# Performance work log

Hardware: AMD Instinct MI355X
Metric: run time of the kernel (lower is better)

## Reference

```python
import jax, jax.numpy as jnp
import numpy as np

B, T, HID = 1, 2048, 2048
H = 16            # num_heads == num_key_value_heads
D = HID // H      # head_dim == feature_dim == 128
EPS = 1e-5


def _layer_norm(x, eps=1e-5):
    mu = jnp.mean(x, axis=-1, keepdims=True)
    var = jnp.mean((x - mu) ** 2, axis=-1, keepdims=True)
    return (x - mu) * jax.lax.rsqrt(var + eps)


def _feature_map(x, gamma, beta):
    # ReBased feature map, flatten=False (parallel mode): affine then LayerNorm
    return _layer_norm(x * gamma + beta)


def setup_inputs() -> dict:
    key = jax.random.key(0)
    ks = jax.random.split(key, 8)
    s = HID ** -0.5
    return {
        "hidden_states": jax.random.normal(ks[0], (B, T, HID), jnp.float32),
        "Wq": jax.random.normal(ks[1], (HID, HID), jnp.float32) * s,
        "Wk": jax.random.normal(ks[2], (HID, HID), jnp.float32) * s,
        "Wv": jax.random.normal(ks[3], (HID, HID), jnp.float32) * s,
        "Wo": jax.random.normal(ks[4], (HID, HID), jnp.float32) * s,
        "gamma": 1.0 + 0.1 * jax.random.normal(ks[5], (D,), jnp.float32),
        "beta": 0.1 * jax.random.normal(ks[6], (D,), jnp.float32),
    }


def reference(hidden_states, Wq, Wk, Wv, Wo, gamma, beta):
    b, t, _ = hidden_states.shape
    # projections (nn.Linear: x @ W.T), split into heads: [b, t, h, d]
    q = (hidden_states @ Wq.T).reshape(b, t, H, D)
    k = (hidden_states @ Wk.T).reshape(b, t, H, D)
    v = (hidden_states @ Wv.T).reshape(b, t, H, D)
    # ReBased feature map (no quadratic flatten in parallel mode)
    q = _feature_map(q, gamma, beta)
    k = _feature_map(k, gamma, beta)
    # parallel_rebased: scale q, quadratic score, causal mask, normalize
    q = q * (D ** -0.5)
    attn = jnp.einsum('bqhd,bkhd->bhqk', q, k) ** 2  # (q.k)^2
    mask = jnp.tril(jnp.ones((t, t), dtype=bool))
    attn = jnp.where(mask, attn, 0.0)
    o = jnp.einsum('bhqk,bkhd->bqhd', attn, v)       # [b, t, h, d]
    z = jnp.sum(attn, axis=-1)                       # [b, h, t]
    o = o / (jnp.swapaxes(z, 1, 2)[..., None] + EPS)
    o = o.reshape(b, t, H * D)
    return o @ Wo.T
```

## Files before the change

kernel.cpp:

```cpp
#include <hip/hip_runtime.h>
#include <hip/hip_bf16.h>
#include <stdint.h>

typedef __bf16 bf16;
typedef __bf16 v8bf __attribute__((ext_vector_type(8)));
typedef float  v4f  __attribute__((ext_vector_type(4)));

#define TSEQ   2048
#define HIDDIM 2048
#define NHEAD  16
#define HDIM   128

__device__ __forceinline__ void async16(void* lds, const void* g)
{
    __builtin_amdgcn_global_load_lds(
        (__attribute__((address_space(1))) void*)(uintptr_t)g,
        (__attribute__((address_space(3))) void*)(unsigned int)(uintptr_t)lds,
        16, 0, 0);
}

__global__ __launch_bounds__(256) void conv5(const float* __restrict__ s0, bf16* __restrict__ d0,
                                             const float* __restrict__ s1, bf16* __restrict__ d1,
                                             const float* __restrict__ s2, bf16* __restrict__ d2,
                                             const float* __restrict__ s3, bf16* __restrict__ d3,
                                             const float* __restrict__ s4, bf16* __restrict__ d4)
{
    const float* src; bf16* dst;
    switch (blockIdx.y) {
        case 0: src = s0; dst = d0; break;
        case 1: src = s1; dst = d1; break;
        case 2: src = s2; dst = d2; break;
        case 3: src = s3; dst = d3; break;
        default: src = s4; dst = d4; break;
    }
    const size_t i = ((size_t)blockIdx.x * 256 + threadIdx.x) * 8;
    const float4 a = *(const float4*)(src + i);
    const float4 b = *(const float4*)(src + i + 4);
    v8bf o;
    o[0] = (bf16)a.x; o[1] = (bf16)a.y; o[2] = (bf16)a.z; o[3] = (bf16)a.w;
    o[4] = (bf16)b.x; o[5] = (bf16)b.y; o[6] = (bf16)b.z; o[7] = (bf16)b.w;
    *(v8bf*)(dst + i) = o;
}


#define PBAR() do { __builtin_amdgcn_sched_barrier(0); __builtin_amdgcn_s_barrier(); \
                    __builtin_amdgcn_sched_barrier(0); } while (0)

#define STU(ldst, gsrc) do { \
    async16((ldst) + w*512,        (gsrc) + (size_t)(w*8 + (l>>3))*2048); \
    async16((ldst) + 4096 + w*512, (gsrc) + (size_t)(64 + w*8 + (l>>3))*2048); \
} while (0)

#define RDA(buf) do { _Pragma("unroll") \
    for (int mi_ = 0; mi_ < 4; ++mi_) { \
        const bf16* p_ = &sA[(buf)*8192 + (wm*64 + mi_*16 + lr)*64]; \
        a[mi_][0] = *(const v8bf*)(p_ + c0); \
        a[mi_][1] = *(const v8bf*)(p_ + c1); } } while (0)

#define RDB(buf, nh) do { _Pragma("unroll") \
    for (int nj_ = 0; nj_ < 2; ++nj_) { \
        const bf16* p_ = &sB[(buf)*24576 + ((nh)*128 + wn*32 + nj_*16 + lr)*64]; \
        b[nj_][0] = *(const v8bf*)(p_ + c0); \
        b[nj_][1] = *(const v8bf*)(p_ + c1); } } while (0)

#define MQ(nh) do { _Pragma("unroll") \
    for (int mi_ = 0; mi_ < 4; ++mi_) { _Pragma("unroll") \
        for (int nj_ = 0; nj_ < 2; ++nj_) { \
            acc[mi_][(nh)*2+nj_] = __builtin_amdgcn_mfma_f32_16x16x32_bf16( \
                a[mi_][0], b[nj_][0], acc[mi_][(nh)*2+nj_], 0, 0, 0); \
            acc[mi_][(nh)*2+nj_] = __builtin_amdgcn_mfma_f32_16x16x32_bf16( \
                a[mi_][1], b[nj_][1], acc[mi_][(nh)*2+nj_], 0, 0, 0); \
        } } } while (0)

#define VMC(n) asm volatile("s_waitcnt vmcnt(" #n ")" ::: "memory")

__global__ __launch_bounds__(512, 2) void gemm_qkv384(const bf16* __restrict__ A,
    const bf16* __restrict__ Wcat, bf16* __restrict__ qb, bf16* __restrict__ kb,
    bf16* __restrict__ vb)
{
    __shared__ __attribute__((aligned(16))) bf16 sA[2*8192];
    __shared__ __attribute__((aligned(16))) bf16 sB[2*24576];
    const int n0g = blockIdx.x * 384;
    const int m0  = blockIdx.y * 128;

    const int tid = threadIdx.x, l = tid & 63, w = tid >> 6;
    const int wm = w >> 2, wn = w & 3;
    const int quad = l >> 4, lr = l & 15;
    const int scol = ((l & 7) ^ ((l >> 3) & 7)) * 8;
    const int c0 = ((quad    ) ^ (lr & 7)) * 8;
    const int c1 = ((quad + 4) ^ (lr & 7)) * 8;

    const bf16* Ag = A    + (size_t)m0  * 2048 + scol;
    const bf16* Bg = Wcat + (size_t)n0g * 2048 + scol;

    v4f  acc[4][6] = {};
    v8bf a[4][2], b[2][2];

    STU(&sA[0],           Ag);
    STU(&sB[0],           Bg);
    STU(&sB[8192],        Bg + (size_t)128*2048);
    STU(&sB[16384],       Bg + (size_t)256*2048);
    STU(&sA[8192],        Ag + 64);
    STU(&sB[24576],       Bg + 64);
    STU(&sB[24576+8192],  Bg + (size_t)128*2048 + 64);
    VMC(10);
    __builtin_amdgcn_s_barrier();
    __builtin_amdgcn_sched_barrier(0);

#pragma unroll 1
    for (int it = 0; it < 16; ++it) {
        const int k1 =  it*128 + 64;
        const int k2 = (it*128 + 128) & 2047;
        const int k3 = (it*128 + 192) & 2047;

        RDA(0); RDB(0, 0);
        STU(&sB[24576+16384], Bg + (size_t)256*2048 + k1);
        PBAR(); __builtin_amdgcn_s_setprio(1); MQ(0); __builtin_amdgcn_s_setprio(0);
        VMC(10); PBAR();
        RDB(0, 1);
        STU(&sA[0], Ag + k2);
        STU(&sB[0], Bg + k2);
        PBAR(); __builtin_amdgcn_s_setprio(1); MQ(1); __builtin_amdgcn_s_setprio(0);
        VMC(12); PBAR();
        RDB(0, 2);
        STU(&sB[8192], Bg + (size_t)128*2048 + k2);
        PBAR(); __builtin_amdgcn_s_setprio(1); MQ(2); __builtin_amdgcn_s_setprio(0);
        VMC(10); PBAR();
        RDA(1); RDB(1, 0);
        STU(&sB[16384], Bg + (size_t)256*2048 + k2);
        PBAR(); __builtin_amdgcn_s_setprio(1); MQ(0); __builtin_amdgcn_s_setprio(0);
        VMC(10); PBAR();
        RDB(1, 1);
        STU(&sA[8192],  Ag + k3);
        STU(&sB[24576], Bg + k3);
        PBAR(); __builtin_amdgcn_s_setprio(1); MQ(1); __builtin_amdgcn_s_setprio(0);
        VMC(12); PBAR();
        RDB(1, 2);
        STU(&sB[24576+8192], Bg + (size_t)128*2048 + k3);
        PBAR(); __builtin_amdgcn_s_setprio(1); MQ(2); __builtin_amdgcn_s_setprio(0);
        VMC(10); PBAR();
    }
    asm volatile("s_waitcnt vmcnt(0)" ::: "memory");

#pragma unroll
    for (int mi = 0; mi < 4; ++mi) {
        const int row = m0 + wm*64 + mi*16 + quad*4;
#pragma unroll
        for (int j = 0; j < 6; ++j) {
            const int colg  = n0g + (j >> 1)*128 + wn*32 + (j & 1)*16;
            const int which = colg >> 11;
            bf16* Cb = (which == 0) ? qb : (which == 1) ? kb : vb;
            const int lcol = (colg & 2047) + lr;
#pragma unroll
            for (int r = 0; r < 4; ++r)
                Cb[(size_t)(row + r)*2048 + lcol] = (bf16)acc[mi][j][r];
        }
    }
}

__global__ __launch_bounds__(256) void gemm_out(const bf16* __restrict__ A,
    const bf16* __restrict__ B, float* __restrict__ C)
{
    __shared__ __attribute__((aligned(16))) bf16 sA[128*32];
    __shared__ __attribute__((aligned(16))) bf16 sB[64*32];
    const int m0 = blockIdx.y * 128, n0 = blockIdx.x * 64;
    const int K = HIDDIM, ldc = HIDDIM;
    const int tid  = threadIdx.x;
    const int lane = tid & 63;
    const int w    = tid >> 6;
    const int wm   = w >> 1, wn = w & 1;
    const int quad = lane >> 4, lr = lane & 15;
    const int srow = lane >> 2;
    const int scol = (lane & 3) * 8;

    const bf16* gA0 = A + (size_t)(m0 + w*32 + srow) * K + scol;
    const bf16* gB0 = B + (size_t)(n0 + w*16 + srow) * K + scol;
    bf16* lA0 = &sA[w*1024];
    bf16* lB0 = &sB[w*512];

    v4f acc[4][2] = {};

    for (int kt = 0; kt < K; kt += 32) {
        __syncthreads();
        async16(lA0,       gA0 + kt);
        async16(lA0 + 512, gA0 + (size_t)16*K + kt);
        async16(lB0,       gB0 + kt);
        __syncthreads();
        v8bf a[4], b[2];
#pragma unroll
        for (int i = 0; i < 4; ++i)
            a[i] = *(const v8bf*)&sA[(wm*64 + i*16 + lr)*32 + quad*8];
#pragma unroll
        for (int j = 0; j < 2; ++j)
            b[j] = *(const v8bf*)&sB[(wn*32 + j*16 + lr)*32 + quad*8];
#pragma unroll
        for (int i = 0; i < 4; ++i)
#pragma unroll
            for (int j = 0; j < 2; ++j)
                acc[i][j] = __builtin_amdgcn_mfma_f32_16x16x32_bf16(a[i], b[j], acc[i][j], 0, 0, 0);
    }

#pragma unroll
    for (int i = 0; i < 4; ++i) {
        const int row_b = m0 + wm*64 + i*16 + quad*4;
#pragma unroll
        for (int j = 0; j < 2; ++j) {
            const int col = n0 + wn*32 + j*16 + lr;
#pragma unroll
            for (int r = 0; r < 4; ++r)
                C[(size_t)(row_b + r)*ldc + col] = acc[i][j][r];
        }
    }
}

__global__ __launch_bounds__(256) void fmap(bf16* __restrict__ qb, bf16* __restrict__ kb,
                                            const float* __restrict__ gamma,
                                            const float* __restrict__ beta)
{
    const int rid  = blockIdx.x * 4 + (threadIdx.x >> 6);
    const int lane = threadIdx.x & 63;
    bf16* base = (rid < TSEQ*NHEAD) ? (qb + (size_t)rid * HDIM)
                                    : (kb + (size_t)(rid - TSEQ*NHEAD) * HDIM);
    const float scale = (rid < TSEQ*NHEAD) ? 0.08838834764831845f : 1.0f;

    const bf16 x0b = base[lane*2], x1b = base[lane*2+1];
    const float g0 = gamma[lane*2], g1 = gamma[lane*2+1];
    const float b0 = beta[lane*2],  b1 = beta[lane*2+1];
    float x0 = (float)x0b*g0 + b0;
    float x1 = (float)x1b*g1 + b1;
    float s  = x0 + x1;
    float sq = x0*x0 + x1*x1;
#pragma unroll
    for (int off = 1; off < 64; off <<= 1) { s += __shfl_xor(s, off); sq += __shfl_xor(sq, off); }
    const float mu   = s * (1.0f/128.0f);
    float var        = sq * (1.0f/128.0f) - mu*mu;
    var = fmaxf(var, 0.0f);
    const float rstd = rsqrtf(var + 1e-5f);
    base[lane*2]   = (bf16)((x0 - mu) * rstd * scale);
    base[lane*2+1] = (bf16)((x1 - mu) * rstd * scale);
}

__global__ __launch_bounds__(256) void transpose2048(const bf16* __restrict__ src,
                                                     bf16* __restrict__ dst)
{
    __shared__ __attribute__((aligned(16))) bf16 tile[64][72];
    const int t0 = blockIdx.y * 64, c0 = blockIdx.x * 64;
    const int tid = threadIdx.x;
    const int r = tid >> 3;
    const int c = (tid & 7) * 8;
#pragma unroll
    for (int p = 0; p < 2; ++p) {
        const int rr = r + p*32;
        *(v8bf*)&tile[rr][c] = *(const v8bf*)(src + (size_t)(t0+rr)*HIDDIM + c0 + c);
    }
    __syncthreads();
#pragma unroll
    for (int p = 0; p < 2; ++p) {
        const int orow = r + p*32;
        v8bf o;
#pragma unroll
        for (int i = 0; i < 8; ++i) o[i] = tile[c + i][orow];
        *(v8bf*)(dst + (size_t)(c0+orow)*HIDDIM + t0 + c) = o;
    }
}

__global__ __launch_bounds__(512, 2) void attn(const bf16* __restrict__ qb,
                                               const bf16* __restrict__ kb,
                                               const bf16* __restrict__ vt,
                                               bf16* __restrict__ ob)
{
    __shared__ __attribute__((aligned(16))) bf16 sK[2*64*136];
    __shared__ __attribute__((aligned(16))) bf16 sV[2*128*72];
    __shared__ __attribute__((aligned(16))) bf16 sS[2*64*72];
    __shared__ __attribute__((aligned(16))) float sO[64*129];
    __shared__ __attribute__((aligned(16))) float sZ[64*17];

    const int h    = blockIdx.y;
    const int pr   = blockIdx.x;
    const int tid  = threadIdx.x, lane = tid & 63;
    const int w    = tid >> 6;
    const int g    = w >> 2;
    const int ww   = w & 3;
    const int quad = lane >> 4, lr = lane & 15;
    const int rs   = tid >> 4;
    const int cs   = (tid & 15) * 8;

#pragma unroll
    for (int ti = 0; ti < 2; ++ti) {
        const int tile = ti ? pr : (31 - pr);
        const int nch  = tile + 1;

        v8bf qa[4];
        {
            const bf16* q0 = qb + (size_t)(tile*64 + ww*16 + lr)*HIDDIM + h*HDIM + quad*8;
#pragma unroll
            for (int ks = 0; ks < 4; ++ks)
                qa[ks] = *(const v8bf*)(q0 + ks*32);
        }

        v4f  o[8] = {};
        float z[4] = {0.f, 0.f, 0.f, 0.f};

        v8bf curK[4], curV[4], nxtK[4], nxtV[4];
#pragma unroll
        for (int p = 0; p < 4; ++p) {
            curK[p] = *(const v8bf*)(kb + (size_t)(rs + p*32)*HIDDIM + h*HDIM + cs);
            curV[p] = *(const v8bf*)(vt + (size_t)(h*HDIM + rs + p*32)*HIDDIM + cs);
        }

        for (int ich = 0; ich < nch; ich += 2) {
            __syncthreads();
#pragma unroll
            for (int p = 0; p < 4; ++p) {
                const int r = rs + p*32;
                *(v8bf*)&sK[(r>>6)*8704 + (r&63)*136 + cs] = curK[p];
            }
#pragma unroll
            for (int p = 0; p < 4; ++p)
                *(v8bf*)&sV[(cs>>6)*9216 + (rs + p*32)*72 + (cs & 63)] = curV[p];

            if (ich + 2 < nch) {
                const int s1 = (ich + 2) * 64;
#pragma unroll
                for (int p = 0; p < 4; ++p) {
                    nxtK[p] = *(const v8bf*)(kb + (size_t)(s1 + rs + p*32)*HIDDIM + h*HDIM + cs);
                    nxtV[p] = *(const v8bf*)(vt + (size_t)(h*HDIM + rs + p*32)*HIDDIM + s1 + cs);
                }
            }
            __syncthreads();

            const int ch = ich + g;
            if (ch < nch) {
                const bf16* sKg = &sK[g*8704];
                const bf16* sVg = &sV[g*9216];
                bf16*       sSg = &sS[g*4608];
                const bool  diag = (ch == tile);
                const int   s0   = ch * 64;

                v8bf kbf[4][4];
#pragma unroll
                for (int nj = 0; nj < 4; ++nj)
#pragma unroll
                    for (int ks = 0; ks < 4; ++ks)
                        kbf[nj][ks] = *(const v8bf*)&sKg[(nj*16 + lr)*136 + ks*32 + quad*8];
                const int row_l = ww*16 + quad*4;
                const int qg    = tile*64 + row_l;
#pragma unroll
                for (int nj = 0; nj < 4; ++nj) {
                    v4f s4 = {0.f, 0.f, 0.f, 0.f};
#pragma unroll
                    for (int ks = 0; ks < 4; ++ks)
                        s4 = __builtin_amdgcn_mfma_f32_16x16x32_bf16(qa[ks], kbf[nj][ks], s4, 0, 0, 0);
                    const int col = nj*16 + lr;
                    const int sg  = s0 + col;
#pragma unroll
                    for (int r = 0; r < 4; ++r) {
                        float val = s4[r] * s4[r];
                        if (diag && (sg > qg + r)) val = 0.0f;
                        const bf16 vb16 = (bf16)val;
                        z[r] += (float)vb16;
                        sSg[(row_l + r)*72 + col] = vb16;
                    }
                }

#pragma unroll
                for (int ks = 0; ks < 2; ++ks) {
                    const v8bf sa = *(const v8bf*)&sSg[(ww*16 + lr)*72 + ks*32 + quad*8];
#pragma unroll
                    for (int nd = 0; nd < 8; ++nd) {
                        const v8bf vbf = *(const v8bf*)&sVg[(nd*16 + lr)*72 + ks*32 + quad*8];
                        o[nd] = __builtin_amdgcn_mfma_f32_16x16x32_bf16(sa, vbf, o[nd], 0, 0, 0);
                    }
                }
            }

            if (ich + 2 < nch) {
#pragma unroll
                for (int p = 0; p < 4; ++p) { curK[p] = nxtK[p]; curV[p] = nxtV[p]; }
            }
        }

        const int row_l = ww*16 + quad*4;
        __syncthreads();
        if (g == 1) {
#pragma unroll
            for (int nd = 0; nd < 8; ++nd)
#pragma unroll
                for (int r = 0; r < 4; ++r)
                    sO[(row_l + r)*129 + nd*16 + lr] = o[nd][r];
#pragma unroll
            for (int r = 0; r < 4; ++r)
                sZ[(row_l + r)*17 + lr] = z[r];
        }
        __syncthreads();
        if (g == 0) {
#pragma unroll
            for (int nd = 0; nd < 8; ++nd)
#pragma unroll
                for (int r = 0; r < 4; ++r)
                    o[nd][r] += sO[(row_l + r)*129 + nd*16 + lr];
#pragma unroll
            for (int r = 0; r < 4; ++r) {
                float zz = z[r] + sZ[(row_l + r)*17 + lr];
                zz += __shfl_xor(zz, 1); zz += __shfl_xor(zz, 2);
                zz += __shfl_xor(zz, 4); zz += __shfl_xor(zz, 8);
                z[r] = zz + 1e-5f;
            }
            const size_t rbase = (size_t)(tile*64 + row_l)*HIDDIM + h*HDIM;
#pragma unroll
            for (int nd = 0; nd < 8; ++nd) {
                const int col = nd*16 + lr;
#pragma unroll
                for (int r = 0; r < 4; ++r)
                    ob[rbase + (size_t)r*HIDDIM + col] = (bf16)(o[nd][r] / z[r]);
            }
        }
    }
}

extern "C" void kernel_launch(void* const* d_in, const int* in_sizes, int n_in,
                              void* d_out, int out_size, void* d_ws, size_t ws_size,
                              hipStream_t stream)
{
    const float* hs    = (const float*)d_in[0];
    const float* Wq    = (const float*)d_in[1];
    const float* Wk    = (const float*)d_in[2];
    const float* Wv    = (const float*)d_in[3];
    const float* Wo    = (const float*)d_in[4];
    const float* gamma = (const float*)d_in[5];
    const float* beta  = (const float*)d_in[6];
    float* outp = (float*)d_out;

    const size_t MAT = (size_t)TSEQ * HIDDIM;

    bf16* ws   = (bf16*)d_ws;
    bf16* hs_b = ws + 0*MAT;
    bf16* vt   = hs_b;
    bf16* Wq_b = ws + 1*MAT;
    bf16* Wk_b = ws + 2*MAT;
    bf16* Wv_b = ws + 3*MAT;
    bf16* Wo_b = ws + 4*MAT;
    bf16* vb   = ws + 5*MAT;
    bf16* ob   = vb;
    bf16* qb   = (bf16*)d_out;
    bf16* kb   = (bf16*)d_out + MAT;

    conv5<<<dim3(2048, 5), 256, 0, stream>>>(hs, hs_b, Wq, Wq_b, Wk, Wk_b, Wv, Wv_b, Wo, Wo_b);
    gemm_qkv384<<<dim3(16, 16), 512, 0, stream>>>(hs_b, Wq_b, qb, kb, vb);
    fmap<<<dim3(2*TSEQ*NHEAD/4), 256, 0, stream>>>(qb, kb, gamma, beta);
    transpose2048<<<dim3(32, 32), 256, 0, stream>>>(vb, vt);
    attn<<<dim3(16, 16), 512, 0, stream>>>(qb, kb, vt, ob);
    gemm_out<<<dim3(32, 16), 256, 0, stream>>>(ob, Wo_b, outp);
}
```

Measured before the change: 269.4 us.

## Fuse feature-map LayerNorm and V transpose into QKV GEMM epilogue

The QKV projection epilogue now applies the affine-plus-LayerNorm feature map to Q and K tiles, using shuffle reductions and an LDS cross-wave reduction over each 128-wide head. It also writes V directly in transposed layout. This removes the separate fmap and transpose kernels together with their global memory round trips and launches. In exchange the GEMM epilogue gains extra LDS traffic and syncs, and the transposed V stores are strided 8-byte writes.

```diff
diff --git a/kernel.cpp b/kernel.cpp
--- a/kernel.cpp
+++ b/kernel.cpp
@@ -4,6 +4,7 @@
 
 typedef __bf16 bf16;
 typedef __bf16 v8bf __attribute__((ext_vector_type(8)));
+typedef __bf16 v4bf __attribute__((ext_vector_type(4)));
 typedef float  v4f  __attribute__((ext_vector_type(4)));
 
 #define TSEQ   2048
@@ -76,7 +77,7 @@
 
 __global__ __launch_bounds__(512, 2) void gemm_qkv384(const bf16* __restrict__ A,
     const bf16* __restrict__ Wcat, bf16* __restrict__ qb, bf16* __restrict__ kb,
-    bf16* __restrict__ vb)
+    bf16* __restrict__ vt, const float* __restrict__ gamma, const float* __restrict__ beta)
 {
     __shared__ __attribute__((aligned(16))) bf16 sA[2*8192];
     __shared__ __attribute__((aligned(16))) bf16 sB[2*24576];
@@ -141,19 +142,88 @@
         VMC(10); PBAR();
     }
     asm volatile("s_waitcnt vmcnt(0)" ::: "memory");
+    __syncthreads();
+
+    float* sRed = (float*)sA;
+    const float g0f = gamma[wn*32 + lr],      b0f = beta[wn*32 + lr];
+    const float g1f = gamma[wn*32 + 16 + lr], b1f = beta[wn*32 + 16 + lr];
+
+#pragma unroll
+    for (int nh = 0; nh < 3; ++nh) {
+        if (((n0g + nh*128) >> 11) == 2) continue;
+#pragma unroll
+        for (int mi = 0; mi < 4; ++mi) {
+            float s[4] = {0.f,0.f,0.f,0.f}, sq[4] = {0.f,0.f,0.f,0.f};
+#pragma unroll
+            for (int jj = 0; jj < 2; ++jj) {
+                const float gg = jj ? g1f : g0f, bb = jj ? b1f : b0f;
+#pragma unroll
+                for (int r = 0; r < 4; ++r) {
+                    float x = acc[mi][nh*2+jj][r] * gg + bb;
+                    acc[mi][nh*2+jj][r] = x;
+                    s[r] += x; sq[r] += x*x;
+                }
+            }
+#pragma unroll
+            for (int off = 1; off < 16; off <<= 1)
+#pragma unroll
+                for (int r = 0; r < 4; ++r) {
+                    s[r]  += __shfl_xor(s[r],  off);
+                    sq[r] += __shfl_xor(sq[r], off);
+                }
+            if (lr == 0) {
+#pragma unroll
+                for (int r = 0; r < 4; ++r) {
+                    const int row = wm*64 + mi*16 + quad*4 + r;
+                    float* p = &sRed[((nh*128 + row)*5 + wn)*2];
+                    p[0] = s[r]; p[1] = sq[r];
+                }
+            }
+        }
+    }
+    __syncthreads();
 
 #pragma unroll
     for (int mi = 0; mi < 4; ++mi) {
         const int row = m0 + wm*64 + mi*16 + quad*4;
-#pragma unroll
-        for (int j = 0; j < 6; ++j) {
-            const int colg  = n0g + (j >> 1)*128 + wn*32 + (j & 1)*16;
+        const int rl0 = wm*64 + mi*16 + quad*4;
+#pragma unroll
+        for (int nh = 0; nh < 3; ++nh) {
+            const int colg  = n0g + nh*128 + wn*32;
             const int which = colg >> 11;
-            bf16* Cb = (which == 0) ? qb : (which == 1) ? kb : vb;
-            const int lcol = (colg & 2047) + lr;
-#pragma unroll
-            for (int r = 0; r < 4; ++r)
-                Cb[(size_t)(row + r)*2048 + lcol] = (bf16)acc[mi][j][r];
+            if (which == 2) {
+#pragma unroll
+                for (int jj = 0; jj < 2; ++jj) {
+                    const int c = (colg & 2047) + jj*16 + lr;
+                    v4bf pk;
+#pragma unroll
+                    for (int r = 0; r < 4; ++r) pk[r] = (bf16)acc[mi][nh*2+jj][r];
+                    *(v4bf*)(vt + (size_t)c*2048 + row) = pk;
+                }
+            } else {
+                bf16* Cb = (which == 0) ? qb : kb;
+                const float qs = (which == 0) ? 0.08838834764831845f : 1.0f;
+#pragma unroll
+                for (int r = 0; r < 4; ++r) {
+                    const int rl = rl0 + r;
+                    float S = 0.f, Q = 0.f;
+#pragma unroll
+                    for (int t = 0; t < 4; ++t) {
+                        const float* p = &sRed[((nh*128 + rl)*5 + t)*2];
+                        S += p[0]; Q += p[1];
+                    }
+                    const float mu = S * (1.0f/128.0f);
+                    float var = Q * (1.0f/128.0f) - mu*mu;
+                    var = fmaxf(var, 0.0f);
+                    const float rstd = rsqrtf(var + 1e-5f) * qs;
+#pragma unroll
+                    for (int jj = 0; jj < 2; ++jj) {
+                        const int lcol = (colg & 2047) + jj*16 + lr;
+                        Cb[(size_t)(row + r)*2048 + lcol] =
+                            (bf16)((acc[mi][nh*2+jj][r] - mu) * rstd);
+                    }
+                }
+            }
         }
     }
 }
@@ -213,57 +283,6 @@
     }
 }
 
-__global__ __launch_bounds__(256) void fmap(bf16* __restrict__ qb, bf16* __restrict__ kb,
-                                            const float* __restrict__ gamma,
-                                            const float* __restrict__ beta)
-{
-    const int rid  = blockIdx.x * 4 + (threadIdx.x >> 6);
-    const int lane = threadIdx.x & 63;
-    bf16* base = (rid < TSEQ*NHEAD) ? (qb + (size_t)rid * HDIM)
-                                    : (kb + (size_t)(rid - TSEQ*NHEAD) * HDIM);
-    const float scale = (rid < TSEQ*NHEAD) ? 0.08838834764831845f : 1.0f;
-
-    const bf16 x0b = base[lane*2], x1b = base[lane*2+1];
-    const float g0 = gamma[lane*2], g1 = gamma[lane*2+1];
-    const float b0 = beta[lane*2],  b1 = beta[lane*2+1];
-    float x0 = (float)x0b*g0 + b0;
-    float x1 = (float)x1b*g1 + b1;
-    float s  = x0 + x1;
-    float sq = x0*x0 + x1*x1;
-#pragma unroll
-    for (int off = 1; off < 64; off <<= 1) { s += __shfl_xor(s, off); sq += __shfl_xor(sq, off); }
-    const float mu   = s * (1.0f/128.0f);
-    float var        = sq * (1.0f/128.0f) - mu*mu;
-    var = fmaxf(var, 0.0f);
-    const float rstd = rsqrtf(var + 1e-5f);
-    base[lane*2]   = (bf16)((x0 - mu) * rstd * scale);
-    base[lane*2+1] = (bf16)((x1 - mu) * rstd * scale);
-}
-
-__global__ __launch_bounds__(256) void transpose2048(const bf16* __restrict__ src,
-                                                     bf16* __restrict__ dst)
-{
-    __shared__ __attribute__((aligned(16))) bf16 tile[64][72];
-    const int t0 = blockIdx.y * 64, c0 = blockIdx.x * 64;
-    const int tid = threadIdx.x;
-    const int r = tid >> 3;
-    const int c = (tid & 7) * 8;
-#pragma unroll
-    for (int p = 0; p < 2; ++p) {
-        const int rr = r + p*32;
-        *(v8bf*)&tile[rr][c] = *(const v8bf*)(src + (size_t)(t0+rr)*HIDDIM + c0 + c);
-    }
-    __syncthreads();
-#pragma unroll
-    for (int p = 0; p < 2; ++p) {
-        const int orow = r + p*32;
-        v8bf o;
-#pragma unroll
-        for (int i = 0; i < 8; ++i) o[i] = tile[c + i][orow];
-        *(v8bf*)(dst + (size_t)(c0+orow)*HIDDIM + t0 + c) = o;
-    }
-}
-
 __global__ __launch_bounds__(512, 2) void attn(const bf16* __restrict__ qb,
                                                const bf16* __restrict__ kb,
                                                const bf16* __restrict__ vt,
@@ -435,20 +454,17 @@
 
     bf16* ws   = (bf16*)d_ws;
     bf16* hs_b = ws + 0*MAT;
-    bf16* vt   = hs_b;
+    bf16* ob   = hs_b;
     bf16* Wq_b = ws + 1*MAT;
     bf16* Wk_b = ws + 2*MAT;
     bf16* Wv_b = ws + 3*MAT;
     bf16* Wo_b = ws + 4*MAT;
-    bf16* vb   = ws + 5*MAT;
-    bf16* ob   = vb;
+    bf16* vt   = ws + 5*MAT;
     bf16* qb   = (bf16*)d_out;
     bf16* kb   = (bf16*)d_out + MAT;
 
     conv5<<<dim3(2048, 5), 256, 0, stream>>>(hs, hs_b, Wq, Wq_b, Wk, Wk_b, Wv, Wv_b, Wo, Wo_b);
-    gemm_qkv384<<<dim3(16, 16), 512, 0, stream>>>(hs_b, Wq_b, qb, kb, vb);
-    fmap<<<dim3(2*TSEQ*NHEAD/4), 256, 0, stream>>>(qb, kb, gamma, beta);
-    transpose2048<<<dim3(32, 32), 256, 0, stream>>>(vb, vt);
+    gemm_qkv384<<<dim3(16, 16), 512, 0, stream>>>(hs_b, Wq_b, qb, kb, vt, gamma, beta);
     attn<<<dim3(16, 16), 512, 0, stream>>>(qb, kb, vt, ob);
     gemm_out<<<dim3(32, 16), 256, 0, stream>>>(ob, Wo_b, outp);
 }
```

Result: no change. 266.8 us (-1.0%).
